# Kernel optimization log

Measured on AMD Instinct MI355X. Metric: run time of the kernel, lower is better.

The kernel has to match this reference:

```python
import jax, jax.numpy as jnp
import numpy as np

E, H, L, B = 2048, 32, 1024, 4
S = E // H  # 64
DM, DD = 32, 64


def _ln(x, w, b, eps=1e-5):
    m = x.mean(-1, keepdims=True)
    v = ((x - m) ** 2).mean(-1, keepdims=True)
    return (x - m) / jnp.sqrt(v + eps) * w + b


def setup_inputs() -> dict:
    key = jax.random.key(0)
    ks = jax.random.split(key, 24)
    sc = 0.02  # weight scale for stability
    d = {
        'x': jax.random.normal(ks[0], (B, L, E), jnp.float32),
        'state': jax.random.normal(ks[1], (B, 2 + S, E), jnp.float32) * 0.1,
        'ln1_w': jnp.ones((E,), jnp.float32), 'ln1_b': jnp.zeros((E,), jnp.float32),
        'ln2_w': jnp.ones((E,), jnp.float32), 'ln2_b': jnp.zeros((E,), jnp.float32),
        'maa_x': jax.random.normal(ks[2], (E,), jnp.float32) * 0.1,
        'maa_w1': jax.random.normal(ks[3], (E, 5 * DM), jnp.float32) * sc,
        'maa_w2': jax.random.normal(ks[4], (5, DM, E), jnp.float32) * sc,
        'maa_stack': jax.random.normal(ks[5], (1, 5, E), jnp.float32) * 0.1,
        'time_decay': jax.random.normal(ks[6], (E,), jnp.float32) * 0.5,
        'td_w1': jax.random.normal(ks[7], (E, DD), jnp.float32) * sc,
        'td_w2': jax.random.normal(ks[8], (DD, E), jnp.float32) * sc,
        'u': jax.random.normal(ks[9], (H, S, 1), jnp.float32) * 0.1,
        'Wr': jax.random.normal(ks[10], (E, E), jnp.float32) * sc,
        'Wk': jax.random.normal(ks[11], (E, E), jnp.float32) * sc,
        'Wv': jax.random.normal(ks[12], (E, E), jnp.float32) * sc,
        'Wg': jax.random.normal(ks[13], (E, E), jnp.float32) * sc,
        'Wo': jax.random.normal(ks[14], (E, E), jnp.float32) * sc,
        'gn_w': jnp.ones((E,), jnp.float32), 'gn_b': jnp.zeros((E,), jnp.float32),
        'ffn_maa_k': jax.random.normal(ks[15], (E,), jnp.float32) * 0.1,
        'ffn_maa_r': jax.random.normal(ks[16], (E,), jnp.float32) * 0.1,
        'Wfk': jax.random.normal(ks[17], (E, E), jnp.float32) * sc,
        'Wfr': jax.random.normal(ks[18], (E, E), jnp.float32) * sc,
        'Wfv': jax.random.normal(ks[19], (E, E), jnp.float32) * sc,
    }
    return d


def _block(x, state, ln1_w, ln1_b, ln2_w, ln2_b, maa_x, maa_w1, maa_w2, maa_stack,
           time_decay, td_w1, td_w2, u, Wr, Wk, Wv, Wg, Wo, gn_w, gn_b,
           ffn_maa_k, ffn_maa_r, Wfk, Wfr, Wfv):
    b, l, e = x.shape
    h = u.shape[0]
    s_ = e // h
    # ---- time mixing (parallel over L, sequential WKV scan) ----
    xa = _ln(x, ln1_w, ln1_b)
    # token shift: sx[t] = x[t-1] - x[t], seeded from state row 1
    sx = jnp.concatenate([state[:, 1:2] - xa[:, :1], xa[:, :-1] - xa[:, 1:]], axis=1)
    xxx = jnp.tanh((xa + sx * maa_x) @ maa_w1).reshape(b, l, 5, DM)
    xxx = jnp.einsum('blfd,fde->blfe', xxx, maa_w2)            # [B,L,5,E]
    xm = xa[:, :, None] + sx[:, :, None] * (maa_stack + xxx)   # [B,L,5,E]
    xk, xw, xv, xr, xg = (xm[:, :, j] for j in range(5))       # stack order: k,w,v,r,g
    w = jnp.exp(-jnp.exp(time_decay + jnp.tanh(xw @ td_w1) @ td_w2)).reshape(b, l, h, s_)
    r = (xr @ Wr.T).reshape(b, l, h, s_)
    k = (xk @ Wk.T).reshape(b, l, h, s_)
    v = (xv @ Wv.T).reshape(b, l, h, s_)
    g = jax.nn.silu(xg @ Wg.T)                                 # [B,L,E]
    s0 = state[:, 2:2 + s_].reshape(b, h, s_, s_)              # per-head WKV state

    def step(s, rkvw):
        r_t, k_t, v_t, w_t = rkvw                              # each [B,H,S]
        a = k_t[..., :, None] * v_t[..., None, :]              # outer product [B,H,S,S]
        out = jnp.einsum('bhi,bhij->bhj', r_t, u * a + s)      # [B,H,S]
        s = a + w_t[..., :, None] * s
        return s, out

    rkvw = tuple(jnp.moveaxis(t, 1, 0) for t in (r, k, v, w))  # [L,B,H,S]
    _, out = jax.lax.scan(step, s0, rkvw)
    out = jnp.moveaxis(out, 0, 1).reshape(b, l, e)             # [B,L,E]
    # group norm over heads (eps=1e-5)
    og = out.reshape(b, l, h, s_)
    m = og.mean(-1, keepdims=True)
    va = ((og - m) ** 2).mean(-1, keepdims=True)
    og = ((og - m) / jnp.sqrt(va + 1e-5)).reshape(b, l, e) * gn_w + gn_b
    x1 = x + (og * g) @ Wo.T
    # ---- channel mixing ----
    xc = _ln(x1, ln2_w, ln2_b)
    sx2 = jnp.concatenate([state[:, 0:1] - xc[:, :1], xc[:, :-1] - xc[:, 1:]], axis=1)
    xk2 = xc + sx2 * ffn_maa_k
    xr2 = xc + sx2 * ffn_maa_r
    rr = jax.nn.sigmoid(xr2 @ Wfr.T)
    kk = jnp.square(jax.nn.relu(xk2 @ Wfk.T))
    return x1 + rr * (kk @ Wfv.T)


def reference(x, state, ln1_w, ln1_b, ln2_w, ln2_b, maa_x, maa_w1, maa_w2, maa_stack,
              time_decay, td_w1, td_w2, u, Wr, Wk, Wv, Wg, Wo, gn_w, gn_b,
              ffn_maa_k, ffn_maa_r, Wfk, Wfr, Wfv):
    return _block(x, state, ln1_w, ln1_b, ln2_w, ln2_b, maa_x, maa_w1, maa_w2, maa_stack,
                  time_decay, td_w1, td_w2, u, Wr, Wk, Wv, Wg, Wo, gn_w, gn_b,
                  ffn_maa_k, ffn_maa_r, Wfk, Wfr, Wfv)
```

## Files before the change

kernel.cpp:

```cpp
#include <hip/hip_runtime.h>


#define E     2048
#define LL    1024
#define HHH   32
#define SSS   64
#define NBL   4096
#define NBLE  8388608

typedef short bf16x8 __attribute__((ext_vector_type(8)));
typedef float f32x4  __attribute__((ext_vector_type(4)));
using u16 = unsigned short;

__device__ __forceinline__ u16 f2b(float f) {
    union { float f; unsigned int u; } c; c.f = f;
    unsigned int u = c.u;
    unsigned int r = (u + 0x7fffu + ((u >> 16) & 1u)) >> 16;
    return (u16)r;
}
__device__ __forceinline__ float b2f(u16 b) {
    union { unsigned int u; float f; } c; c.u = ((unsigned int)b) << 16; return c.f;
}

__device__ __forceinline__ float wave_sum(float v) {
#pragma unroll
    for (int m = 32; m >= 1; m >>= 1) v += __shfl_xor(v, m, 64);
    return v;
}

__device__ __forceinline__ void gl_lds16(const void* g, void* l) {
    __builtin_amdgcn_global_load_lds((const __attribute__((address_space(1))) unsigned int*)g,
                                     (__attribute__((address_space(3))) unsigned int*)l, 16, 0, 0);
}

template <int CTRL>
__device__ __forceinline__ float dpp_mov(float v) {
    int s = __builtin_bit_cast(int, v);
    int r = __builtin_amdgcn_update_dpp(s, s, CTRL, 0xF, 0xF, false);
    return __builtin_bit_cast(float, r);
}


__global__ __launch_bounds__(256) void k_convert(const float* __restrict__ in,
                                                 u16* __restrict__ out, int n) {
    int i = (blockIdx.x * 256 + threadIdx.x) * 4;
    if (i >= n) return;
    float4 v = *reinterpret_cast<const float4*>(in + i);
    ushort4 o = make_ushort4(f2b(v.x), f2b(v.y), f2b(v.z), f2b(v.w));
    *reinterpret_cast<ushort4*>(out + i) = o;
}

__global__ __launch_bounds__(256) void k_transpose(const float* __restrict__ in,
                                                   u16* __restrict__ out, int R, int C) {
    int i = blockIdx.x * 256 + threadIdx.x;
    if (i >= R * C) return;
    int r = i / C, c = i - r * C;
    out[c * R + r] = f2b(in[i]);
}

__global__ __launch_bounds__(256) void k_ln(const float* __restrict__ x,
                                            const float* __restrict__ w,
                                            const float* __restrict__ b,
                                            float* __restrict__ out) {
    int row = blockIdx.x, tid = threadIdx.x;
    const float* xr = x + (size_t)row * E + tid * 8;
    float4 v0 = *reinterpret_cast<const float4*>(xr);
    float4 v1 = *reinterpret_cast<const float4*>(xr + 4);
    float s = v0.x + v0.y + v0.z + v0.w + v1.x + v1.y + v1.z + v1.w;
    __shared__ float red[4];
    s = wave_sum(s);
    int wid = tid >> 6, lane = tid & 63;
    if (lane == 0) red[wid] = s;
    __syncthreads();
    float mean = (red[0] + red[1] + red[2] + red[3]) * (1.0f / E);
    __syncthreads();
    float q = 0.f;
    q += (v0.x - mean) * (v0.x - mean); q += (v0.y - mean) * (v0.y - mean);
    q += (v0.z - mean) * (v0.z - mean); q += (v0.w - mean) * (v0.w - mean);
    q += (v1.x - mean) * (v1.x - mean); q += (v1.y - mean) * (v1.y - mean);
    q += (v1.z - mean) * (v1.z - mean); q += (v1.w - mean) * (v1.w - mean);
    q = wave_sum(q);
    if (lane == 0) red[wid] = q;
    __syncthreads();
    float inv = rsqrtf((red[0] + red[1] + red[2] + red[3]) * (1.0f / E) + 1e-5f);
    int e = tid * 8;
    float4 w0 = *reinterpret_cast<const float4*>(w + e);
    float4 w1 = *reinterpret_cast<const float4*>(w + e + 4);
    float4 b0 = *reinterpret_cast<const float4*>(b + e);
    float4 b1 = *reinterpret_cast<const float4*>(b + e + 4);
    float4 o0, o1;
    o0.x = (v0.x - mean) * inv * w0.x + b0.x; o0.y = (v0.y - mean) * inv * w0.y + b0.y;
    o0.z = (v0.z - mean) * inv * w0.z + b0.z; o0.w = (v0.w - mean) * inv * w0.w + b0.w;
    o1.x = (v1.x - mean) * inv * w1.x + b1.x; o1.y = (v1.y - mean) * inv * w1.y + b1.y;
    o1.z = (v1.z - mean) * inv * w1.z + b1.z; o1.w = (v1.w - mean) * inv * w1.w + b1.w;
    float* op = out + (size_t)row * E + e;
    *reinterpret_cast<float4*>(op) = o0;
    *reinterpret_cast<float4*>(op + 4) = o1;
}

__global__ __launch_bounds__(256) void k_mk(const float* __restrict__ xa,
                                            const float* __restrict__ state,
                                            const float* __restrict__ maa_x,
                                            u16* __restrict__ out) {
    int i = (blockIdx.x * 256 + threadIdx.x) * 4;
    if (i >= NBLE) return;
    int n = i >> 11, e = i & (E - 1);
    int l = n & (LL - 1), b = n >> 10;
    float4 cur = *reinterpret_cast<const float4*>(xa + i);
    float4 prev;
    if (l > 0) prev = *reinterpret_cast<const float4*>(xa + i - E);
    else       prev = *reinterpret_cast<const float4*>(state + (size_t)b * 66 * E + E + e);
    float4 m = *reinterpret_cast<const float4*>(maa_x + e);
    ushort4 o = make_ushort4(f2b(cur.x + (prev.x - cur.x) * m.x),
                             f2b(cur.y + (prev.y - cur.y) * m.y),
                             f2b(cur.z + (prev.z - cur.z) * m.z),
                             f2b(cur.w + (prev.w - cur.w) * m.w));
    *reinterpret_cast<ushort4*>(out + i) = o;
}

__global__ __launch_bounds__(256) void k_mix2(const float* __restrict__ xc,
                                              const float* __restrict__ state,
                                              const float* __restrict__ mk,
                                              const float* __restrict__ mr,
                                              u16* __restrict__ xk2,
                                              u16* __restrict__ xr2) {
    int i = (blockIdx.x * 256 + threadIdx.x) * 4;
    if (i >= NBLE) return;
    int n = i >> 11, e = i & (E - 1);
    int l = n & (LL - 1), b = n >> 10;
    float4 cur = *reinterpret_cast<const float4*>(xc + i);
    float4 prev;
    if (l > 0) prev = *reinterpret_cast<const float4*>(xc + i - E);
    else       prev = *reinterpret_cast<const float4*>(state + (size_t)b * 66 * E + e);
    float4 sx = make_float4(prev.x - cur.x, prev.y - cur.y, prev.z - cur.z, prev.w - cur.w);
    float4 k4 = *reinterpret_cast<const float4*>(mk + e);
    float4 r4 = *reinterpret_cast<const float4*>(mr + e);
    ushort4 ok = make_ushort4(f2b(cur.x + sx.x * k4.x), f2b(cur.y + sx.y * k4.y),
                              f2b(cur.z + sx.z * k4.z), f2b(cur.w + sx.w * k4.w));
    ushort4 orr = make_ushort4(f2b(cur.x + sx.x * r4.x), f2b(cur.y + sx.y * r4.y),
                               f2b(cur.z + sx.z * r4.z), f2b(cur.w + sx.w * r4.w));
    *reinterpret_cast<ushort4*>(xk2 + i) = ok;
    *reinterpret_cast<ushort4*>(xr2 + i) = orr;
}

__global__ __launch_bounds__(256) void k_gnorm(const float* __restrict__ wkv,
                                               const u16* __restrict__ g,
                                               const float* __restrict__ gw,
                                               const float* __restrict__ gb,
                                               u16* __restrict__ ogg) {
    int gidx = blockIdx.x * 4 + (threadIdx.x >> 6);
    int lane = threadIdx.x & 63;
    int n = gidx >> 5, h = gidx & 31;
    size_t base = (size_t)n * E + h * SSS;
    float v = wkv[base + lane];
    float mean = wave_sum(v) * (1.0f / SSS);
    float d = v - mean;
    float var = wave_sum(d * d) * (1.0f / SSS);
    float norm = d * rsqrtf(var + 1e-5f);
    int e = h * SSS + lane;
    float res = norm * gw[e] + gb[e];
    float gv = b2f(g[base + lane]);
    ogg[base + lane] = f2b(res * gv);
}

#define CT 16

__global__ __launch_bounds__(256) void k_scan(const u16* __restrict__ Rb,
                                              const u16* __restrict__ Kb,
                                              const u16* __restrict__ Vb,
                                              const float* __restrict__ W,
                                              const float* __restrict__ state,
                                              const float* __restrict__ u,
                                              float* __restrict__ out) {
    __shared__ u16   ldsR[2][CT * 64];
    __shared__ u16   ldsK[2][CT * 64];
    __shared__ float ldsW[2][CT * 64];
    __shared__ u16   ldsV[2][CT * 16];
    const int blk = blockIdx.x;
    const int bh = blk & 127;
    const int jq = blk >> 7;
    const int b = bh >> 5, h = bh & 31;
    const int tid = threadIdx.x;
    const int wvid = tid >> 6;
    const int lane = tid & 63;
    const int ig = (lane & 3) | (((lane >> 4) & 3) << 2);
    const int jl = (lane >> 2) & 3;
    const int jv = wvid * 4 + jl;
    const int j  = jq * 16 + jv;
    const int i0 = ig * 4;
    float s[4], uu[4];
    const float* s0 = state + (size_t)b * 66 * E + 2 * E + h * (SSS * SSS);
#pragma unroll
    for (int ii = 0; ii < 4; ii++) {
        s[ii] = s0[(i0 + ii) * SSS + j];
        uu[ii] = u[h * SSS + i0 + ii];
    }
    const size_t off0 = (size_t)b * LL * E + h * SSS;

    auto stage = [&](int c, int bufsel) {
        size_t base = off0 + (size_t)c * CT * E;
        if (wvid == 0) {
            const u16* g0 = Rb + base + (size_t)(lane >> 3) * E + ((lane & 7) << 3);
            gl_lds16(g0,         &ldsR[bufsel][lane * 8]);
            gl_lds16(g0 + 8 * E, &ldsR[bufsel][512 + lane * 8]);
            if (lane < 32) {
                const u16* gv = Vb + base + (size_t)(lane >> 1) * E + jq * 16 + ((lane & 1) << 3);
                gl_lds16(gv, &ldsV[bufsel][lane * 8]);
            }
        } else if (wvid == 1) {
            const u16* g0 = Kb + base + (size_t)(lane >> 3) * E + ((lane & 7) << 3);
            gl_lds16(g0,         &ldsK[bufsel][lane * 8]);
            gl_lds16(g0 + 8 * E, &ldsK[bufsel][512 + lane * 8]);
        } else if (wvid == 2) {
            const float* g0 = W + base + (size_t)(lane >> 4) * E + ((lane & 15) << 2);
            gl_lds16(g0,         &ldsW[bufsel][lane * 4]);
            gl_lds16(g0 + 4 * E, &ldsW[bufsel][256 + lane * 4]);
        } else {
            const float* g0 = W + base + (size_t)(8 + (lane >> 4)) * E + ((lane & 15) << 2);
            gl_lds16(g0,         &ldsW[bufsel][512 + lane * 4]);
            gl_lds16(g0 + 4 * E, &ldsW[bufsel][768 + lane * 4]);
        }
    };

    stage(0, 0);
    __syncthreads();
    int cur = 0;
    for (int c = 0; c < LL / CT; c++) {
        if (c + 1 < LL / CT) stage(c + 1, cur ^ 1);
        float accs[CT];
#pragma unroll
        for (int tt = 0; tt < CT; tt++) {
            ushort4 rv = *reinterpret_cast<const ushort4*>(&ldsR[cur][tt * 64 + i0]);
            ushort4 kv = *reinterpret_cast<const ushort4*>(&ldsK[cur][tt * 64 + i0]);
            float4  wv = *reinterpret_cast<const float4*>(&ldsW[cur][tt * 64 + i0]);
            float vj = b2f(ldsV[cur][tt * 16 + jv]);
            float acc = 0.f, a;
            a = b2f(kv.x) * vj; acc += b2f(rv.x) * fmaf(uu[0], a, s[0]); s[0] = fmaf(wv.x, s[0], a);
            a = b2f(kv.y) * vj; acc += b2f(rv.y) * fmaf(uu[1], a, s[1]); s[1] = fmaf(wv.y, s[1], a);
            a = b2f(kv.z) * vj; acc += b2f(rv.z) * fmaf(uu[2], a, s[2]); s[2] = fmaf(wv.z, s[2], a);
            a = b2f(kv.w) * vj; acc += b2f(rv.w) * fmaf(uu[3], a, s[3]); s[3] = fmaf(wv.w, s[3], a);
            accs[tt] = acc;
        }
#pragma unroll
        for (int tt = 0; tt < CT; tt++) accs[tt] += dpp_mov<0xB1>(accs[tt]);
#pragma unroll
        for (int tt = 0; tt < CT; tt++) accs[tt] += dpp_mov<0x4E>(accs[tt]);
#pragma unroll
        for (int tt = 0; tt < CT; tt++) accs[tt] += __shfl_xor(accs[tt], 16, 64);
#pragma unroll
        for (int tt = 0; tt < CT; tt++) accs[tt] += __shfl_xor(accs[tt], 32, 64);
        if (ig == 0) {
            size_t offt = off0 + (size_t)c * CT * E + j;
#pragma unroll
            for (int tt = 0; tt < CT; tt++) out[offt + (size_t)tt * E] = accs[tt];
        }
        __syncthreads();
        cur ^= 1;
    }
}

template <int EP>
__global__ __launch_bounds__(512, 2) void k_gemm256(const u16* __restrict__ A,
                                                    const u16* __restrict__ Bw,
                                                    void* __restrict__ C,
                                                    const float* __restrict__ emat1,
                                                    const float* __restrict__ emat2) {
    __shared__ u16 As[3][256 * 64];
    __shared__ u16 Bs[3][128 * 64];
    const int tid = threadIdx.x;
    const int bid = blockIdx.x;
    const int sw = (bid & 7) * 32 + (bid >> 3);
    const int m0 = (sw >> 4) << 8;
    const int n0 = (sw & 15) << 7;
    const int srow = tid >> 3;
    const int schunk = (tid & 7) ^ (srow & 7);
    const u16* gA = A + (size_t)(m0 + srow) * E + schunk * 8;
    const u16* gB = Bw + (size_t)(n0 + srow) * E + schunk * 8;

    const int wv = tid >> 6, lane = tid & 63;
    const int wm = wv >> 1, wn = wv & 1;
    const int lr = lane & 15, lq = lane >> 4;
    const int c0 = ((lq ^ (lr & 7)) << 3);
    const int c1 = (((4 + lq) ^ (lr & 7)) << 3);
    const int arow = wm * 64 + lr;
    const int brow = wn * 64 + lr;

    f32x4 acc[4][4];
#pragma unroll
    for (int mt = 0; mt < 4; mt++)
#pragma unroll
        for (int nt = 0; nt < 4; nt++) acc[mt][nt] = {0.f, 0.f, 0.f, 0.f};

    const int NT = E / 64;

    auto stage_full = [&](int kt, int buf) {
        const u16* a = gA + kt * 64;
        const u16* b = gB + kt * 64;
        u16* la = &As[buf][0] + tid * 8;
        u16* lb = &Bs[buf][0] + tid * 8;
        gl_lds16(a,                   la);
        gl_lds16(a + (size_t)64  * E, la + 64 * 64);
        gl_lds16(a + (size_t)128 * E, la + 128 * 64);
        gl_lds16(a + (size_t)192 * E, la + 192 * 64);
        gl_lds16(b,                   lb);
        gl_lds16(b + (size_t)64  * E, lb + 64 * 64);
    };

    stage_full(0, 0);
    stage_full(1, 1);
    asm volatile("s_waitcnt vmcnt(6)" ::: "memory");
    __builtin_amdgcn_s_barrier();

    for (int kt = 0; kt < NT; kt++) {
        const int rb = kt % 3;
        const int sb = (kt + 2) % 3;
        const bool st = (kt + 2) < NT;
        const u16* as = &As[rb][0];
        const u16* bs = &Bs[rb][0];
        const u16* ga = gA + (kt + 2) * 64;
        const u16* gb = gB + (kt + 2) * 64;
        u16* la = &As[sb][0] + tid * 8;
        u16* lb = &Bs[sb][0] + tid * 8;
        bf16x8 a0[4], a1[4], b0[4], b1[4];

        #pragma unroll
        for (int mt = 0; mt < 4; mt++)
            a0[mt] = *reinterpret_cast<const bf16x8*>(as + (arow + mt * 16) * 64 + c0);
        #pragma unroll
        for (int nt = 0; nt < 4; nt++)
            b0[nt] = *reinterpret_cast<const bf16x8*>(bs + (brow + nt * 16) * 64 + c0);
        if (st) {
            gl_lds16(ga,                   la);
            gl_lds16(ga + (size_t)64  * E, la + 64 * 64);
            gl_lds16(ga + (size_t)128 * E, la + 128 * 64);
        }
        __builtin_amdgcn_s_barrier();
        asm volatile("s_waitcnt lgkmcnt(0)" ::: "memory");
        __builtin_amdgcn_s_setprio(1);
        #pragma unroll
        for (int mt = 0; mt < 4; mt++)
            #pragma unroll
            for (int nt = 0; nt < 4; nt++)
                acc[mt][nt] = __builtin_amdgcn_mfma_f32_16x16x32_bf16(a0[mt], b0[nt], acc[mt][nt], 0, 0, 0);
        __builtin_amdgcn_s_setprio(0);
        __builtin_amdgcn_s_barrier();

        #pragma unroll
        for (int mt = 0; mt < 4; mt++)
            a1[mt] = *reinterpret_cast<const bf16x8*>(as + (arow + mt * 16) * 64 + c1);
        #pragma unroll
        for (int nt = 0; nt < 4; nt++)
            b1[nt] = *reinterpret_cast<const bf16x8*>(bs + (brow + nt * 16) * 64 + c1);
        if (st) {
            gl_lds16(ga + (size_t)192 * E, la + 192 * 64);
            gl_lds16(gb,                   lb);
            gl_lds16(gb + (size_t)64  * E, lb + 64 * 64);
            asm volatile("s_waitcnt vmcnt(6)" ::: "memory");
        } else {
            asm volatile("s_waitcnt vmcnt(0)" ::: "memory");
        }
        __builtin_amdgcn_s_barrier();
        asm volatile("s_waitcnt lgkmcnt(0)" ::: "memory");
        __builtin_amdgcn_s_setprio(1);
        #pragma unroll
        for (int mt = 0; mt < 4; mt++)
            #pragma unroll
            for (int nt = 0; nt < 4; nt++)
                acc[mt][nt] = __builtin_amdgcn_mfma_f32_16x16x32_bf16(a1[mt], b1[nt], acc[mt][nt], 0, 0, 0);
        __builtin_amdgcn_s_setprio(0);
        __builtin_amdgcn_s_barrier();
    }

    const int gmb = m0 + wm * 64 + (lq << 2);
    const int gnb = n0 + wn * 64 + lr;
#pragma unroll
    for (int mt = 0; mt < 4; mt++) {
#pragma unroll
        for (int nt = 0; nt < 4; nt++) {
            int gn = gnb + nt * 16;
#pragma unroll
            for (int i = 0; i < 4; i++) {
                int gm = gmb + mt * 16 + i;
                size_t idx = (size_t)gm * E + gn;
                float v = acc[mt][nt][i];
                if constexpr (EP == 5) ((float*)C)[idx] = emat1[idx] + v;
                else if constexpr (EP == 6) ((float*)C)[idx] = 1.f / (1.f + expf(-v));
                else if constexpr (EP == 7) { float t = fmaxf(v, 0.f); ((u16*)C)[idx] = f2b(t * t); }
                else if constexpr (EP == 8) ((float*)C)[idx] = emat1[idx] + emat2[idx] * v;
                else if constexpr (EP == 9) ((u16*)C)[idx] = f2b(v);
                else if constexpr (EP == 10) { float sg = 1.f / (1.f + expf(-v)); ((u16*)C)[idx] = f2b(v * sg); }
            }
        }
    }
}

template <int EP>
__global__ __launch_bounds__(256) void k_gemm128(const u16* __restrict__ A, int lda,
                                                 const u16* __restrict__ Bw,
                                                 void* __restrict__ C, int K,
                                                 const float* __restrict__ evec,
                                                 const float* __restrict__ emat1,
                                                 const float* __restrict__ emat2) {
    __shared__ u16 As[128 * 32];
    __shared__ u16 Bs[128 * 32];
    const int tid = threadIdx.x;
    const int m0 = blockIdx.y << 7, n0 = blockIdx.x << 7;
    const int srow = tid >> 2;
    const int scol = (((tid & 3) ^ ((srow >> 1) & 3)) << 3);
    const int wv = tid >> 6, lane = tid & 63;
    const int wy = (wv >> 1) << 6, wx = (wv & 1) << 6;
    const int lr = lane & 15, lq = lane >> 4;
    const int cofs = ((lq ^ ((lr >> 1) & 3)) << 3);
    f32x4 acc[4][4];
#pragma unroll
    for (int a = 0; a < 4; a++)
#pragma unroll
        for (int bq = 0; bq < 4; bq++) acc[a][bq] = {0.f, 0.f, 0.f, 0.f};
    const u16* gA = A + (size_t)(m0 + srow) * lda + scol;
    const u16* gB = Bw + (size_t)(n0 + srow) * K + scol;
    u16* lA = As + srow * 32 + ((tid & 3) << 3);
    u16* lB = Bs + srow * 32 + ((tid & 3) << 3);
    for (int k0 = 0; k0 < K; k0 += 32) {
        gl_lds16(gA + k0, lA);
        gl_lds16(gA + (size_t)64 * lda + k0, lA + 64 * 32);
        gl_lds16(gB + k0, lB);
        gl_lds16(gB + (size_t)64 * K + k0, lB + 64 * 32);
        __syncthreads();
        bf16x8 af[4], bfr[4];
#pragma unroll
        for (int mt = 0; mt < 4; mt++)
            af[mt] = *reinterpret_cast<const bf16x8*>(As + (wy + mt * 16 + lr) * 32 + cofs);
#pragma unroll
        for (int nt = 0; nt < 4; nt++)
            bfr[nt] = *reinterpret_cast<const bf16x8*>(Bs + (wx + nt * 16 + lr) * 32 + cofs);
#pragma unroll
        for (int mt = 0; mt < 4; mt++)
#pragma unroll
            for (int nt = 0; nt < 4; nt++)
                acc[mt][nt] = __builtin_amdgcn_mfma_f32_16x16x32_bf16(af[mt], bfr[nt], acc[mt][nt], 0, 0, 0);
        __syncthreads();
    }
    const int gmb = m0 + wy + (lq << 2);
    const int gnb = n0 + wx + lr;
#pragma unroll
    for (int mt = 0; mt < 4; mt++) {
#pragma unroll
        for (int nt = 0; nt < 4; nt++) {
            int gn = gnb + nt * 16;
#pragma unroll
            for (int i = 0; i < 4; i++) {
                int gm = gmb + mt * 16 + i;
                size_t idx = (size_t)gm * E + gn;
                float v = acc[mt][nt][i];
                if constexpr (EP == 2) {
                    int l = gm & (LL - 1), bb = gm >> 10;
                    float cur = emat1[idx];
                    float prev = (l > 0) ? emat1[idx - E]
                                         : emat2[(size_t)bb * 66 * E + E + gn];
                    ((u16*)C)[idx] = f2b(cur + (prev - cur) * (evec[gn] + v));
                }
                else if constexpr (EP == 3) ((float*)C)[idx] = expf(-expf(evec[gn] + v));
            }
        }
    }
}

#define BK  32
#define LDP 40

template <int EP>
__global__ __launch_bounds__(256) void k_gemm(const u16* __restrict__ A, int lda,
                                              const u16* __restrict__ Bw,
                                              void* __restrict__ C,
                                              int M, int N, int K) {
    __shared__ u16 As[64 * LDP];
    __shared__ u16 Bs[64 * LDP];
    const int tid = threadIdx.x;
    const int m0 = blockIdx.y << 6, n0 = blockIdx.x << 6;
    const int srow = tid >> 2, skc = (tid & 3) << 3;
    const int lane = tid & 63, wv = tid >> 6;
    const int wr = (wv >> 1) << 5, wc = (wv & 1) << 5;
    const int lr = lane & 15, lq = lane >> 4;
    f32x4 acc[2][2];
#pragma unroll
    for (int a = 0; a < 2; a++)
#pragma unroll
        for (int bq = 0; bq < 2; bq++) acc[a][bq] = {0.f, 0.f, 0.f, 0.f};
    const u16* aptr = A + (size_t)(m0 + srow) * lda + skc;
    const u16* bptr = Bw + (size_t)(n0 + srow) * K + skc;
    const bool bvalid = (n0 + srow) < N;
    for (int k0 = 0; k0 < K; k0 += BK) {
        float4 av = *reinterpret_cast<const float4*>(aptr + k0);
        float4 bv = bvalid ? *reinterpret_cast<const float4*>(bptr + k0)
                           : make_float4(0.f, 0.f, 0.f, 0.f);
        __syncthreads();
        *reinterpret_cast<float4*>(As + srow * LDP + skc) = av;
        *reinterpret_cast<float4*>(Bs + srow * LDP + skc) = bv;
        __syncthreads();
        bf16x8 a0 = *reinterpret_cast<const bf16x8*>(As + (wr + lr) * LDP + lq * 8);
        bf16x8 a1 = *reinterpret_cast<const bf16x8*>(As + (wr + 16 + lr) * LDP + lq * 8);
        bf16x8 b0 = *reinterpret_cast<const bf16x8*>(Bs + (wc + lr) * LDP + lq * 8);
        bf16x8 b1 = *reinterpret_cast<const bf16x8*>(Bs + (wc + 16 + lr) * LDP + lq * 8);
        acc[0][0] = __builtin_amdgcn_mfma_f32_16x16x32_bf16(a0, b0, acc[0][0], 0, 0, 0);
        acc[0][1] = __builtin_amdgcn_mfma_f32_16x16x32_bf16(a0, b1, acc[0][1], 0, 0, 0);
        acc[1][0] = __builtin_amdgcn_mfma_f32_16x16x32_bf16(a1, b0, acc[1][0], 0, 0, 0);
        acc[1][1] = __builtin_amdgcn_mfma_f32_16x16x32_bf16(a1, b1, acc[1][1], 0, 0, 0);
    }
    const int gmb = m0 + wr + lq * 4;
    const int gnb = n0 + wc + lr;
#pragma unroll
    for (int mi = 0; mi < 2; mi++) {
#pragma unroll
        for (int ni = 0; ni < 2; ni++) {
            int gn = gnb + ni * 16;
            if (gn >= N) continue;
#pragma unroll
            for (int i = 0; i < 4; i++) {
                int gm = gmb + mi * 16 + i;
                size_t idx = (size_t)gm * N + gn;
                float v = acc[mi][ni][i];
                if constexpr (EP == 1) ((u16*)C)[idx] = f2b(tanhf(v));
            }
        }
    }
}


extern "C" void kernel_launch(void* const* d_in, const int* in_sizes, int n_in,
                              void* d_out, int out_size, void* d_ws, size_t ws_size,
                              hipStream_t stream) {
    const float* x          = (const float*)d_in[0];
    const float* state      = (const float*)d_in[1];
    const float* ln1_w      = (const float*)d_in[2];
    const float* ln1_b      = (const float*)d_in[3];
    const float* ln2_w      = (const float*)d_in[4];
    const float* ln2_b      = (const float*)d_in[5];
    const float* maa_x      = (const float*)d_in[6];
    const float* maa_w1     = (const float*)d_in[7];
    const float* maa_w2     = (const float*)d_in[8];
    const float* maa_stack  = (const float*)d_in[9];
    const float* time_decay = (const float*)d_in[10];
    const float* td_w1      = (const float*)d_in[11];
    const float* td_w2      = (const float*)d_in[12];
    const float* u          = (const float*)d_in[13];
    const float* Wr         = (const float*)d_in[14];
    const float* Wk         = (const float*)d_in[15];
    const float* Wv         = (const float*)d_in[16];
    const float* Wg         = (const float*)d_in[17];
    const float* Wo         = (const float*)d_in[18];
    const float* gn_w       = (const float*)d_in[19];
    const float* gn_b       = (const float*)d_in[20];
    const float* ffn_k      = (const float*)d_in[21];
    const float* ffn_r      = (const float*)d_in[22];
    const float* Wfk        = (const float*)d_in[23];
    const float* Wfr        = (const float*)d_in[24];
    const float* Wfv        = (const float*)d_in[25];

    char* ws = (char*)d_ws;
    float* R0 = (float*)(ws);
    float* R1 = (float*)(ws + 33554432);
    u16*   R2 = (u16*)(ws + 67108864);
    u16*   R3 = (u16*)(ws + 83886080);
    u16*   R4 = (u16*)(ws + 100663296);
    u16*   R5 = (u16*)(ws + 117440512);
    u16*   R6 = (u16*)(ws + 134217728);
    u16*   WB = (u16*)(ws + 150994944);
    u16*   Hx = (u16*)(ws + 159383552);
    u16*   Ht = (u16*)(ws + 160694272);
    u16*  WT1 = (u16*)(ws + 161218560);
    u16*  WT2 = (u16*)(ws + 161873920);
    u16*  WT3 = (u16*)(ws + 162529280);
    u16*  WT4 = (u16*)(ws + 162791424);

    dim3 blk(256);
    dim3 blk512(512);
    dim3 g256(256);
    dim3 g128(16, 32);
    dim3 g160(3, 64), g64(1, 64);
    const int ncv = (E * E / 4) / 256;
    const int nel = NBLE / 1024;

    k_transpose<<<(E * 160 + 255) / 256, blk, 0, stream>>>(maa_w1, WT1, E, 160);
    for (int f = 0; f < 5; f++)
        k_transpose<<<(32 * E + 255) / 256, blk, 0, stream>>>(maa_w2 + f * 32 * E, WT2 + f * E * 32, 32, E);
    k_transpose<<<(E * 64 + 255) / 256, blk, 0, stream>>>(td_w1, WT3, E, 64);
    k_transpose<<<(64 * E + 255) / 256, blk, 0, stream>>>(td_w2, WT4, 64, E);

    k_ln<<<NBL, blk, 0, stream>>>(x, ln1_w, ln1_b, R0);
    k_mk<<<nel, blk, 0, stream>>>(R0, state, maa_x, R2);
    k_gemm<1><<<g160, blk, 0, stream>>>(R2, E, WT1, Hx, NBL, 160, E);

    k_gemm128<2><<<g128, blk, 0, stream>>>(Hx + 1 * 32, 160, WT2 + 1 * E * 32, R2, 32,
                                           maa_stack + 1 * E, R0, state);
    k_gemm<1><<<g64, blk, 0, stream>>>(R2, E, WT3, Ht, NBL, 64, E);
    k_gemm128<3><<<g128, blk, 0, stream>>>(Ht, 64, WT4, R1, 64, time_decay, nullptr, nullptr);

    k_gemm128<2><<<g128, blk, 0, stream>>>(Hx + 0 * 32, 160, WT2 + 0 * E * 32, R2, 32,
                                           maa_stack + 0 * E, R0, state);
    k_convert<<<ncv, blk, 0, stream>>>(Wk, WB, E * E);
    k_gemm256<9><<<g256, blk512, 0, stream>>>(R2, WB, R4, nullptr, nullptr);

    k_gemm128<2><<<g128, blk, 0, stream>>>(Hx + 2 * 32, 160, WT2 + 2 * E * 32, R2, 32,
                                           maa_stack + 2 * E, R0, state);
    k_convert<<<ncv, blk, 0, stream>>>(Wv, WB, E * E);
    k_gemm256<9><<<g256, blk512, 0, stream>>>(R2, WB, R5, nullptr, nullptr);

    k_gemm128<2><<<g128, blk, 0, stream>>>(Hx + 4 * 32, 160, WT2 + 4 * E * 32, R2, 32,
                                           maa_stack + 4 * E, R0, state);
    k_convert<<<ncv, blk, 0, stream>>>(Wg, WB, E * E);
    k_gemm256<10><<<g256, blk512, 0, stream>>>(R2, WB, R6, nullptr, nullptr);

    k_gemm128<2><<<g128, blk, 0, stream>>>(Hx + 3 * 32, 160, WT2 + 3 * E * 32, R2, 32,
                                           maa_stack + 3 * E, R0, state);
    k_convert<<<ncv, blk, 0, stream>>>(Wr, WB, E * E);
    k_gemm256<9><<<g256, blk512, 0, stream>>>(R2, WB, R3, nullptr, nullptr);

    k_scan<<<512, blk, 0, stream>>>(R3, R4, R5, R1, state, u, R0);
    k_gnorm<<<NBL * HHH / 4, blk, 0, stream>>>(R0, R6, gn_w, gn_b, R6);

    k_convert<<<ncv, blk, 0, stream>>>(Wo, WB, E * E);
    k_gemm256<5><<<g256, blk512, 0, stream>>>(R6, WB, R0, x, nullptr);

    k_ln<<<NBL, blk, 0, stream>>>(R0, ln2_w, ln2_b, R1);
    k_mix2<<<nel, blk, 0, stream>>>(R1, state, ffn_k, ffn_r, R2, R3);
    k_convert<<<ncv, blk, 0, stream>>>(Wfk, WB, E * E);
    k_gemm256<7><<<g256, blk512, 0, stream>>>(R2, WB, R4, nullptr, nullptr);
    k_convert<<<ncv, blk, 0, stream>>>(Wfr, WB, E * E);
    k_gemm256<6><<<g256, blk512, 0, stream>>>(R3, WB, R1, nullptr, nullptr);
    k_convert<<<ncv, blk, 0, stream>>>(Wfv, WB, E * E);
    k_gemm256<8><<<g256, blk512, 0, stream>>>(R4, WB, (float*)d_out, R0, R1);
}
```

Measured before the change: 962.7 us.

## Restructure GEMM main loop into single-phase triple-buffered pipeline

Replaces the two half-step K loop, which interleaved partial global-to-LDS loads with two MFMA phases and four barriers, with one phase per tile. Each iteration issues the whole stage for tile kt+2, waits with vmcnt(12) for tile kt, reads both K halves from LDS and runs all 32 MFMAs back to back. This cuts barriers per iteration from four to two and issues larger batches of LDS reads. In exchange, LDS reads no longer overlap the preceding MFMA phase, and more A/B fragments are live at once, which raises register pressure.

```diff
diff --git a/kernel.cpp b/kernel.cpp
--- a/kernel.cpp
+++ b/kernel.cpp
@@ -308,67 +308,43 @@
 
     stage_full(0, 0);
     stage_full(1, 1);
-    asm volatile("s_waitcnt vmcnt(6)" ::: "memory");
-    __builtin_amdgcn_s_barrier();
 
     for (int kt = 0; kt < NT; kt++) {
         const int rb = kt % 3;
         const int sb = (kt + 2) % 3;
-        const bool st = (kt + 2) < NT;
-        const u16* as = &As[rb][0];
-        const u16* bs = &Bs[rb][0];
-        const u16* ga = gA + (kt + 2) * 64;
-        const u16* gb = gB + (kt + 2) * 64;
-        u16* la = &As[sb][0] + tid * 8;
-        u16* lb = &Bs[sb][0] + tid * 8;
-        bf16x8 a0[4], a1[4], b0[4], b1[4];
-
-        #pragma unroll
-        for (int mt = 0; mt < 4; mt++)
-            a0[mt] = *reinterpret_cast<const bf16x8*>(as + (arow + mt * 16) * 64 + c0);
-        #pragma unroll
-        for (int nt = 0; nt < 4; nt++)
-            b0[nt] = *reinterpret_cast<const bf16x8*>(bs + (brow + nt * 16) * 64 + c0);
-        if (st) {
-            gl_lds16(ga,                   la);
-            gl_lds16(ga + (size_t)64  * E, la + 64 * 64);
-            gl_lds16(ga + (size_t)128 * E, la + 128 * 64);
-        }
-        __builtin_amdgcn_s_barrier();
-        asm volatile("s_waitcnt lgkmcnt(0)" ::: "memory");
-        __builtin_amdgcn_s_setprio(1);
-        #pragma unroll
-        for (int mt = 0; mt < 4; mt++)
-            #pragma unroll
-            for (int nt = 0; nt < 4; nt++)
-                acc[mt][nt] = __builtin_amdgcn_mfma_f32_16x16x32_bf16(a0[mt], b0[nt], acc[mt][nt], 0, 0, 0);
-        __builtin_amdgcn_s_setprio(0);
-        __builtin_amdgcn_s_barrier();
-
-        #pragma unroll
-        for (int mt = 0; mt < 4; mt++)
-            a1[mt] = *reinterpret_cast<const bf16x8*>(as + (arow + mt * 16) * 64 + c1);
-        #pragma unroll
-        for (int nt = 0; nt < 4; nt++)
-            b1[nt] = *reinterpret_cast<const bf16x8*>(bs + (brow + nt * 16) * 64 + c1);
-        if (st) {
-            gl_lds16(ga + (size_t)192 * E, la + 192 * 64);
-            gl_lds16(gb,                   lb);
-            gl_lds16(gb + (size_t)64  * E, lb + 64 * 64);
+        asm volatile("s_barrier" ::: "memory");
+        if (kt + 2 < NT) {
+            stage_full(kt + 2, sb);
+            asm volatile("s_waitcnt vmcnt(12)" ::: "memory");
+        } else if (kt + 1 < NT) {
             asm volatile("s_waitcnt vmcnt(6)" ::: "memory");
         } else {
             asm volatile("s_waitcnt vmcnt(0)" ::: "memory");
         }
-        __builtin_amdgcn_s_barrier();
+        asm volatile("s_barrier" ::: "memory");
+        const u16* as = &As[rb][0];
+        const u16* bs = &Bs[rb][0];
+        bf16x8 a0[4], a1[4], b0[4], b1[4];
+#pragma unroll
+        for (int mt = 0; mt < 4; mt++) {
+            a0[mt] = *reinterpret_cast<const bf16x8*>(as + (arow + mt * 16) * 64 + c0);
+            a1[mt] = *reinterpret_cast<const bf16x8*>(as + (arow + mt * 16) * 64 + c1);
+        }
+#pragma unroll
+        for (int nt = 0; nt < 4; nt++) {
+            b0[nt] = *reinterpret_cast<const bf16x8*>(bs + (brow + nt * 16) * 64 + c0);
+            b1[nt] = *reinterpret_cast<const bf16x8*>(bs + (brow + nt * 16) * 64 + c1);
+        }
         asm volatile("s_waitcnt lgkmcnt(0)" ::: "memory");
         __builtin_amdgcn_s_setprio(1);
-        #pragma unroll
+#pragma unroll
         for (int mt = 0; mt < 4; mt++)
-            #pragma unroll
-            for (int nt = 0; nt < 4; nt++)
+#pragma unroll
+            for (int nt = 0; nt < 4; nt++) {
+                acc[mt][nt] = __builtin_amdgcn_mfma_f32_16x16x32_bf16(a0[mt], b0[nt], acc[mt][nt], 0, 0, 0);
                 acc[mt][nt] = __builtin_amdgcn_mfma_f32_16x16x32_bf16(a1[mt], b1[nt], acc[mt][nt], 0, 0, 0);
+            }
         __builtin_amdgcn_s_setprio(0);
-        __builtin_amdgcn_s_barrier();
     }
 
     const int gmb = m0 + wm * 64 + (lq << 2);
```

After: 1.024 ms. 1.06x slower.
